# Performance work log

Hardware: AMD Instinct MI355X
Metric: run time of the kernel (lower is better)

The kernel has to match this reference:

```python
import jax, jax.numpy as jnp
import numpy as np

N, E, D, H, ED = 50000, 150000, 128, 4, 16


def _ln(x, g, b, eps=1e-5):
    m = jnp.mean(x, -1, keepdims=True)
    v = jnp.var(x, -1, keepdims=True)
    return (x - m) / jnp.sqrt(v + eps) * g + b


def _seg_softmax(logits, seg, n):
    # numerically stable softmax over edges grouped by destination node
    m = jax.ops.segment_max(logits, seg, num_segments=n)
    e = jnp.exp(logits - m[seg])
    s = jax.ops.segment_sum(e, seg, num_segments=n)
    return e / (s[seg] + 1e-16)


def setup_inputs():
    key = jax.random.key(0)
    ks = jax.random.split(key, 16)
    def w(i, shape, s=0.05):
        return jax.random.normal(ks[i], shape, jnp.float32) * s
    return dict(
        x=w(0, (N, D), 1.0),
        edge_index=jax.random.randint(ks[1], (2, E), 0, N),
        edge_attr=w(2, (E, ED), 1.0),
        sage_Wl=w(3, (D, D)), sage_Wr=w(4, (D, D)), sage_b=jnp.zeros((D,), jnp.float32),
        tq_W=w(5, (D, H * D)), tq_b=jnp.zeros((H * D,), jnp.float32),
        tk_W=w(6, (D, H * D)), tk_b=jnp.zeros((H * D,), jnp.float32),
        tv_W=w(7, (D, H * D)), tv_b=jnp.zeros((H * D,), jnp.float32),
        te_W=w(8, (ED, H * D)),
        tskip_W=w(9, (D, D)), tskip_b=jnp.zeros((D,), jnp.float32),
        gat_W=w(10, (D, H * D)), gat_att_src=w(11, (H, D)), gat_att_dst=w(12, (H, D)),
        gat_bias=jnp.zeros((D,), jnp.float32),
        gate_short=jnp.ones((1,), jnp.float32), gate_attn=jnp.ones((1,), jnp.float32),
        gate_neighbor=jnp.ones((1,), jnp.float32),
        fus_W=w(13, (3 * D, D)), fus_b=jnp.zeros((D,), jnp.float32),
        fus_g=jnp.ones((D,), jnp.float32), fus_beta=jnp.zeros((D,), jnp.float32),
        norm_g=jnp.ones((D,), jnp.float32), norm_b=jnp.zeros((D,), jnp.float32),
    )


def reference(x, edge_index, edge_attr, sage_Wl, sage_Wr, sage_b,
              tq_W, tq_b, tk_W, tk_b, tv_W, tv_b, te_W, tskip_W, tskip_b,
              gat_W, gat_att_src, gat_att_dst, gat_bias,
              gate_short, gate_attn, gate_neighbor,
              fus_W, fus_b, fus_g, fus_beta, norm_g, norm_b):
    n, d = x.shape
    h = tq_W.shape[1] // d
    src, dst = edge_index[0], edge_index[1]

    # --- SAGEConv: mean aggregation of neighbors + root linear ---
    agg = jax.ops.segment_sum(x[src], dst, num_segments=n)
    cnt = jax.ops.segment_sum(jnp.ones((src.shape[0],), x.dtype), dst, num_segments=n)
    mean = agg / jnp.maximum(cnt, 1.0)[:, None]
    x_short = jax.nn.relu(mean @ sage_Wl + x @ sage_Wr + sage_b)

    # --- TransformerConv (concat=False, edge-conditioned key/value, skip) ---
    q = (x @ tq_W + tq_b).reshape(n, h, d)
    k = (x @ tk_W + tk_b).reshape(n, h, d)
    v = (x @ tv_W + tv_b).reshape(n, h, d)
    e = (edge_attr @ te_W).reshape(-1, h, d)           # [E,H,d]
    logits = jnp.sum(q[dst] * (k[src] + e), -1) / np.float32(np.sqrt(d))  # [E,H]
    alpha = _seg_softmax(logits, dst, n)
    out_t = jax.ops.segment_sum((v[src] + e) * alpha[..., None], dst, num_segments=n).mean(1)
    x_attn = jax.nn.relu(out_t + x @ tskip_W + tskip_b)

    # --- GATConv (adds self-loops, concat=False averages heads, bias) ---
    loops = jnp.arange(n)
    s2 = jnp.concatenate([src, loops])
    d2 = jnp.concatenate([dst, loops])
    g = (x @ gat_W).reshape(n, h, d)
    a_s = jnp.sum(g * gat_att_src, -1)                 # [N,H]
    a_d = jnp.sum(g * gat_att_dst, -1)
    lg = jax.nn.leaky_relu(a_s[s2] + a_d[d2], 0.2)     # [E+N,H]
    al = _seg_softmax(lg, d2, n)
    out_g = jax.ops.segment_sum(g[s2] * al[..., None], d2, num_segments=n).mean(1) + gat_bias
    x_nb = jax.nn.relu(out_g)

    # --- gated fusion + residual LayerNorm ---
    gs = jax.nn.sigmoid(gate_short)
    ga = jax.nn.sigmoid(gate_attn)
    gn = jax.nn.sigmoid(gate_neighbor)
    cat = jnp.concatenate([x_short * gs, x_attn * ga, x_nb * gn], -1)
    fused = jax.nn.relu(_ln(cat @ fus_W + fus_b, fus_g, fus_beta))
    return _ln(x + fused, norm_g, norm_b)
```

## Files before the change

kernel.cpp:

```cpp
#include <hip/hip_runtime.h>
#include <hip/hip_bf16.h>

using bf16 = __hip_bfloat16;
typedef __attribute__((ext_vector_type(8))) short short8;
typedef __attribute__((ext_vector_type(4))) float f32x4;
typedef __attribute__((ext_vector_type(4))) unsigned short u16x4;

__device__ __forceinline__ void store4(bf16* p, float v0, float v1, float v2, float v3) {
    u16x4 pk;
    bf16 h0 = __float2bfloat16(v0); pk[0] = *(unsigned short*)&h0;
    bf16 h1 = __float2bfloat16(v1); pk[1] = *(unsigned short*)&h1;
    bf16 h2 = __float2bfloat16(v2); pk[2] = *(unsigned short*)&h2;
    bf16 h3 = __float2bfloat16(v3); pk[3] = *(unsigned short*)&h3;
    *(u16x4*)p = pk;
}
__device__ __forceinline__ float b2f(short s) { bf16 h; *(short*)&h = s; return __bfloat162float(h); }

__device__ __forceinline__ void ld_lds16(void* lds, const void* g) {
    __builtin_amdgcn_global_load_lds(
        (const __attribute__((address_space(1))) unsigned int*)g,
        (__attribute__((address_space(3))) unsigned int*)lds,
        16, 0, 0);
}

__device__ __forceinline__ size_t pidx(int c, int k, int K) {
    return ((size_t)(((c >> 6) * (K >> 5) + (k >> 5)) * 4 + ((c >> 4) & 3)) * 64
            + (((k >> 3) & 3) * 16 + (c & 15))) * 8 + (k & 7);
}

__global__ __launch_bounds__(256) void zero_ws(unsigned* p, size_t n) {
    size_t i = (size_t)blockIdx.x * 256 + threadIdx.x;
    size_t stride = (size_t)gridDim.x * 256;
    for (; i < n; i += stride) p[i] = 0u;
}

__global__ __launch_bounds__(256) void prep_all(
    const float* __restrict__ x, bf16* __restrict__ x_b,
    bf16* __restrict__ Wt_sage, const float* __restrict__ sage_Wl, const float* __restrict__ sage_Wr,
    bf16* __restrict__ Wt_fus, const float* __restrict__ fus_W,
    const float* __restrict__ gate_s, const float* __restrict__ gate_a, const float* __restrict__ gate_n,
    bf16* __restrict__ Wt_cat, const float* __restrict__ tvW,
    const float* __restrict__ tskipW, const float* __restrict__ teW,
    bf16* __restrict__ Wgag, const float* __restrict__ gatW,
    float* __restrict__ bvsum, const float* __restrict__ tvb, int ND)
{
    const int TP = 128 * 128;
    long i = (long)blockIdx.x * 256 + threadIdx.x;
    long nv = ND >> 3;
    if (i < nv) {
        long b = i * 8;
        f32x4 a0 = *(const f32x4*)(x + b);
        f32x4 a1 = *(const f32x4*)(x + b + 4);
        short8 o;
        #pragma unroll
        for (int j = 0; j < 4; ++j) { bf16 h = __float2bfloat16(a0[j]); o[j] = *(short*)&h; }
        #pragma unroll
        for (int j = 0; j < 4; ++j) { bf16 h = __float2bfloat16(a1[j]); o[4 + j] = *(short*)&h; }
        *(short8*)(x_b + b) = o;
        return;
    }
    i -= nv;
    if (i < TP) { int k = (int)i / 128, c = (int)i % 128; Wt_sage[pidx(c, k, 256)] = __float2bfloat16(sage_Wl[i]); return; }
    i -= TP;
    if (i < TP) { int k = (int)i / 128, c = (int)i % 128; Wt_sage[pidx(c, k + 128, 256)] = __float2bfloat16(sage_Wr[i]); return; }
    i -= TP;
    if (i < 3 * TP) {
        int sseg = (int)(i / TP); int r = (int)(i % TP);
        int k = r / 128, c = r % 128;
        const float* g = sseg == 0 ? gate_s : (sseg == 1 ? gate_a : gate_n);
        float gv = 1.0f / (1.0f + expf(-g[0]));
        Wt_fus[pidx(c, sseg * 128 + k, 384)] = __float2bfloat16(fus_W[(size_t)sseg * TP + r] * gv);
        return;
    }
    i -= 3L * TP;
    if (i < 128L * 704) {
        int d = (int)(i / 704), kk = (int)(i % 704);
        float v;
        if (kk < 512)      { int h = kk >> 7, k = kk & 127; v = 0.25f * tvW[k * 512 + h * 128 + d]; }
        else if (kk < 640) { int k = kk - 512;              v = tskipW[k * 128 + d]; }
        else               { int t = kk - 640; int h = t >> 4, j = t & 15; v = 0.25f * teW[j * 512 + h * 128 + d]; }
        Wt_cat[pidx(d, kk, 704)] = __float2bfloat16(v);
        return;
    }
    i -= 128L * 704;
    if (i < 128L * 512) {
        int d = (int)i >> 9, k = (int)i & 511;
        int h = k >> 7, i2 = k & 127;
        Wgag[pidx(d, k, 512)] = __float2bfloat16(0.25f * gatW[(size_t)i2 * 512 + h * 128 + d]);
        return;
    }
    i -= 128L * 512;
    if (i < 128) {
        int d = (int)i;
        bvsum[d] = 0.25f * (tvb[d] + tvb[128 + d] + tvb[256 + d] + tvb[384 + d]);
    }
}

__global__ __launch_bounds__(128) void build_wbig(
    bf16* __restrict__ Wbig, float* __restrict__ bbig,
    const float* __restrict__ Wq, const float* __restrict__ Wk,
    const float* __restrict__ teW, const float* __restrict__ bq,
    const float* __restrict__ bk, const float* __restrict__ gatW,
    const float* __restrict__ attS, const float* __restrict__ attD)
{
    int c = blockIdx.x;
    int ip = threadIdx.x;
    float acc = 0.f, bacc = 0.f;
    if (c < 512) {
        int h = c >> 7, i2 = c & 127;
        const float* wkrow = Wk + (size_t)i2 * 512 + h * 128;
        const float* wqrow = Wq + (size_t)ip * 512 + h * 128;
        for (int o = 0; o < 128; ++o) acc += wqrow[o] * wkrow[o];
        if (ip == 0) { const float* bqr = bq + h * 128; for (int o = 0; o < 128; ++o) bacc += bqr[o] * wkrow[o]; }
    } else if (c < 576) {
        int t = c - 512; int h = t >> 4, j = t & 15;
        const float* terow = teW + (size_t)j * 512 + h * 128;
        const float* wqrow = Wq + (size_t)ip * 512 + h * 128;
        for (int o = 0; o < 128; ++o) acc += wqrow[o] * terow[o];
        if (ip == 0) { const float* bqr = bq + h * 128; for (int o = 0; o < 128; ++o) bacc += bqr[o] * terow[o]; }
    } else if (c < 580) {
        int h = c - 576;
        const float* bkr = bk + h * 128;
        const float* wqrow = Wq + (size_t)ip * 512 + h * 128;
        for (int o = 0; o < 128; ++o) acc += wqrow[o] * bkr[o];
        if (ip == 0) { const float* bqr = bq + h * 128; for (int o = 0; o < 128; ++o) bacc += bqr[o] * bkr[o]; }
    } else if (c < 584) {
        int h = c - 580;
        const float* ar = attS + h * 128;
        const float* gr = gatW + (size_t)ip * 512 + h * 128;
        for (int d = 0; d < 128; ++d) acc += gr[d] * ar[d];
    } else if (c < 588) {
        int h = c - 584;
        const float* ar = attD + h * 128;
        const float* gr = gatW + (size_t)ip * 512 + h * 128;
        for (int d = 0; d < 128; ++d) acc += gr[d] * ar[d];
    }
    Wbig[pidx(c, ip, 128)] = __float2bfloat16(acc);
    if (ip == 0) bbig[c] = bacc;
}

__global__ __launch_bounds__(256) void k_hist(const int* __restrict__ dst, int* __restrict__ deg_i, int E) {
    int e = blockIdx.x * 256 + threadIdx.x;
    if (e < E) atomicAdd(&deg_i[dst[e]], 1);
}

__global__ __launch_bounds__(256) void k_scan1(
    const int* __restrict__ deg_i, int* __restrict__ loc, int* __restrict__ partial, int N)
{
    __shared__ int sm[256];
    int t = threadIdx.x, i = blockIdx.x * 256 + t;
    int v = (i < N) ? deg_i[i] : 0;
    sm[t] = v;
    __syncthreads();
    for (int off = 1; off < 256; off <<= 1) {
        int add = (t >= off) ? sm[t - off] : 0;
        __syncthreads();
        sm[t] += add;
        __syncthreads();
    }
    if (i < N) loc[i] = sm[t] - v;
    if (t == 255) partial[blockIdx.x] = sm[255];
}

__global__ __launch_bounds__(256) void k_scan2(int* __restrict__ partial, int nb) {
    __shared__ int sm[256];
    int t = threadIdx.x;
    int v = (t < nb) ? partial[t] : 0;
    sm[t] = v;
    __syncthreads();
    for (int off = 1; off < 256; off <<= 1) {
        int add = (t >= off) ? sm[t - off] : 0;
        __syncthreads();
        sm[t] += add;
        __syncthreads();
    }
    if (t < nb) partial[t] = sm[t] - v;
}

__global__ __launch_bounds__(256) void k_scan3(
    const int* __restrict__ loc, const int* __restrict__ partial,
    int* __restrict__ rowptr, int* __restrict__ cursor, int N)
{
    int i = blockIdx.x * 256 + threadIdx.x;
    if (i >= N) return;
    int r = loc[i] + partial[blockIdx.x];
    rowptr[i] = r;
    cursor[i] = r;
}

__global__ __launch_bounds__(256) void k_scatter(
    const int* __restrict__ src, const int* __restrict__ dst,
    int* __restrict__ cursor, int* __restrict__ col_src, int* __restrict__ eidx, int E)
{
    int e = blockIdx.x * 256 + threadIdx.x;
    if (e >= E) return;
    int d = dst[e];
    int pos = atomicAdd(&cursor[d], 1);
    col_src[pos] = src[e];
    eidx[pos] = e;
}

__global__ __launch_bounds__(128) void gemm_wide(
    const bf16* __restrict__ A, const bf16* __restrict__ Wt,
    const float* __restrict__ bias, bf16* __restrict__ C, int n_rows, int ldc)
{
    int row0 = blockIdx.x * 64;
    int wave = threadIdx.x >> 6, lane = threadIdx.x & 63;
    int lrow = lane & 15, quad = lane >> 4;
    short8 xb[4][4];
    #pragma unroll
    for (int ks = 0; ks < 4; ++ks)
        #pragma unroll
        for (int nt = 0; nt < 4; ++nt) {
            int r = row0 + nt * 16 + lrow;
            r = r < n_rows ? r : n_rows - 1;
            xb[ks][nt] = *(const short8*)(A + (size_t)r * 128 + ks * 32 + quad * 8);
        }
    int c64 = blockIdx.y * 2 + wave;
    int cbase = c64 * 64;
    f32x4 acc[4][4] = {};
    #pragma unroll
    for (int ks = 0; ks < 4; ++ks) {
        short8 wf[4];
        #pragma unroll
        for (int mt = 0; mt < 4; ++mt)
            wf[mt] = *(const short8*)(Wt + ((size_t)((c64 * 4 + ks) * 4 + mt) * 64 + lane) * 8);
        #pragma unroll
        for (int mt = 0; mt < 4; ++mt)
            #pragma unroll
            for (int nt = 0; nt < 4; ++nt)
                acc[mt][nt] = __builtin_amdgcn_mfma_f32_16x16x32_bf16(wf[mt], xb[ks][nt], acc[mt][nt], 0, 0, 0);
    }
    #pragma unroll
    for (int nt = 0; nt < 4; ++nt) {
        int row = row0 + nt * 16 + lrow;
        if (row >= n_rows) continue;
        #pragma unroll
        for (int mt = 0; mt < 4; ++mt) {
            int col = cbase + mt * 16 + quad * 4;
            float b0 = 0.f, b1 = 0.f, b2 = 0.f, b3 = 0.f;
            if (bias) { b0 = bias[col]; b1 = bias[col + 1]; b2 = bias[col + 2]; b3 = bias[col + 3]; }
            store4(&C[(size_t)row * ldc + col],
                   acc[mt][nt][0] + b0, acc[mt][nt][1] + b1,
                   acc[mt][nt][2] + b2, acc[mt][nt][3] + b3);
        }
    }
}

#define NCAP 8
__global__ __launch_bounds__(256) void node_fused(
    const bf16* __restrict__ QT, const bf16* __restrict__ x_b,
    const float* __restrict__ edge_attr,
    const int* __restrict__ rowptr, const int* __restrict__ deg_i,
    const int* __restrict__ col_src, const int* __restrict__ eidx,
    bf16* __restrict__ mean_b, bf16* __restrict__ xa, bf16* __restrict__ ga,
    bf16* __restrict__ ea_b, int N)
{
    __shared__ short8 xS[4][NCAP][16];
    __shared__ float eaS[4][NCAP][16];
    __shared__ float wTs[4][NCAP][4];
    __shared__ float wGs[4][NCAP][4];
    int w = threadIdx.x >> 6, l = threadIdx.x & 63;
    int n = blockIdx.x * 4 + w;
    if (n >= N) return;
    int j = l & 15, g4 = l >> 4;
    int p0 = rowptr[n], dg = deg_i[n];
    const float scale = 0.08838834764831845f;
    float qtF[4][8], qeqL[4], qbL[4], adh[4], ashn[4];
    #pragma unroll
    for (int h = 0; h < 4; ++h) {
        short8 q = *(const short8*)(QT + (size_t)n * 640 + h * 128 + j * 8);
        #pragma unroll
        for (int t = 0; t < 8; ++t) qtF[h][t] = b2f(q[t]);
        qeqL[h] = __bfloat162float(QT[(size_t)n * 640 + 512 + h * 16 + j]);
        qbL[h]  = __bfloat162float(QT[(size_t)n * 640 + 576 + h]);
        ashn[h] = __bfloat162float(QT[(size_t)n * 640 + 580 + h]);
        adh[h]  = __bfloat162float(QT[(size_t)n * 640 + 584 + h]);
    }
    float xn0 = __bfloat162float(x_b[(size_t)n * 128 + l]);
    float xn1 = __bfloat162float(x_b[(size_t)n * 128 + l + 64]);
    float s_t[4], s_g[4], xaacc[8] = {}, gaacc[8];
    float mean0 = 0.f, mean1 = 0.f, eaacc = 0.f;
    #pragma unroll
    for (int h = 0; h < 4; ++h) {
        s_t[h] = 0.f;
        float lgs = ashn[h] + adh[h];
        lgs = lgs > 0.f ? lgs : 0.2f * lgs;
        float e = __expf(lgs);
        s_g[h] = e;
        gaacc[h * 2] = e * xn0; gaacc[h * 2 + 1] = e * xn1;
    }
    for (int c0 = 0; c0 < dg; c0 += NCAP) {
        int cc = min(NCAP, dg - c0);
        for (int it = 0; it < ((cc + 3) >> 2); ++it) {
            int i = it * 4 + g4;
            bool valid = i < cc;
            int s = 0;
            short8 xf = {0, 0, 0, 0, 0, 0, 0, 0};
            float ea_j = 0.f;
            if (valid) {
                s = col_src[p0 + c0 + i];
                int eg = eidx[p0 + c0 + i];
                xf = *(const short8*)(x_b + (size_t)s * 128 + j * 8);
                ea_j = edge_attr[(size_t)eg * 16 + j];
                xS[w][i][j] = xf;
                eaS[w][i][j] = ea_j;
            }
            float xv[8];
            #pragma unroll
            for (int t = 0; t < 8; ++t) xv[t] = b2f(xf[t]);
            float p[4];
            #pragma unroll
            for (int h = 0; h < 4; ++h) {
                float a = ea_j * qeqL[h];
                #pragma unroll
                for (int t = 0; t < 8; ++t) a += xv[t] * qtF[h][t];
                p[h] = a;
            }
            #pragma unroll
            for (int off = 1; off < 16; off <<= 1)
                #pragma unroll
                for (int h = 0; h < 4; ++h)
                    p[h] += __shfl_xor(p[h], off, 64);
            if (valid && j == 0) {
                #pragma unroll
                for (int h = 0; h < 4; ++h) {
                    wTs[w][i][h] = __expf((p[h] + qbL[h]) * scale);
                    float as_s = __bfloat162float(QT[(size_t)s * 640 + 580 + h]);
                    float lg = as_s + adh[h];
                    lg = lg > 0.f ? lg : 0.2f * lg;
                    wGs[w][i][h] = __expf(lg);
                }
            }
        }
        for (int i = 0; i < cc; ++i) {
            const bf16* xr = (const bf16*)&xS[w][i][0];
            float xv0 = __bfloat162float(xr[l]);
            float xv1 = __bfloat162float(xr[l + 64]);
            mean0 += xv0; mean1 += xv1;
            #pragma unroll
            for (int h = 0; h < 4; ++h) {
                float at = wTs[w][i][h], ag = wGs[w][i][h];
                s_t[h] += at; s_g[h] += ag;
                xaacc[h * 2] += at * xv0; xaacc[h * 2 + 1] += at * xv1;
                gaacc[h * 2] += ag * xv0; gaacc[h * 2 + 1] += ag * xv1;
            }
            eaacc += wTs[w][i][g4] * eaS[w][i][j];
        }
    }
    float invd = 1.f / fmaxf((float)dg, 1.f);
    mean_b[(size_t)n * 128 + l]      = __float2bfloat16(mean0 * invd);
    mean_b[(size_t)n * 128 + l + 64] = __float2bfloat16(mean1 * invd);
    #pragma unroll
    for (int h = 0; h < 4; ++h) {
        float it = 1.f / (s_t[h] + 1e-16f);
        xa[(size_t)n * 512 + h * 128 + l]      = __float2bfloat16(xaacc[h * 2] * it);
        xa[(size_t)n * 512 + h * 128 + l + 64] = __float2bfloat16(xaacc[h * 2 + 1] * it);
        float ig = 1.f / (s_g[h] + 1e-16f);
        ga[(size_t)n * 512 + h * 128 + l]      = __float2bfloat16(gaacc[h * 2] * ig);
        ga[(size_t)n * 512 + h * 128 + l + 64] = __float2bfloat16(gaacc[h * 2 + 1] * ig);
    }
    ea_b[(size_t)n * 64 + l] = __float2bfloat16(eaacc / (s_t[g4] + 1e-16f));
}

#define STASH(BIASP, USE_BV) do { \
    _Pragma("unroll") \
    for (int nt = 0; nt < 4; ++nt) { \
        int row_l = nt * 16 + lrow; \
        int sw = (row_l & 7) << 4; \
        float bvf = (USE_BV) ? ((deg_i[rA[nt]] > 0) ? 1.f : 0.f) : 0.f; \
        _Pragma("unroll") \
        for (int mt = 0; mt < 4; ++mt) { \
            int col = cbase + mt * 16 + quad * 4; \
            f32x4 bb = *(const f32x4*)((BIASP) + col); \
            u16x4 pk; \
            _Pragma("unroll") \
            for (int jj = 0; jj < 4; ++jj) { \
                float v = acc[mt][nt][jj] + bb[jj]; \
                if (USE_BV) v += bvf * bvsum[col + jj]; \
                bf16 h = __float2bfloat16(fmaxf(v, 0.f)); \
                pk[jj] = *(unsigned short*)&h; \
            } \
            *(u16x4*)(tileb + row_l * 256 + ((col * 2) ^ sw)) = pk; \
        } \
    } \
} while (0)

__global__ __launch_bounds__(128) void tail_fused(
    const bf16* __restrict__ mean_b, const bf16* __restrict__ x_b,
    const bf16* __restrict__ ga, const bf16* __restrict__ xa,
    const bf16* __restrict__ ea_b, const int* __restrict__ deg_i,
    const float* __restrict__ x,
    const bf16* __restrict__ Wt_sage, const bf16* __restrict__ Wgag,
    const bf16* __restrict__ Wt_cat, const bf16* __restrict__ Wt_fus,
    const float* __restrict__ sage_b, const float* __restrict__ gat_bias,
    const float* __restrict__ tskip_b, const float* __restrict__ bvsum,
    const float* __restrict__ fus_b, const float* __restrict__ fus_g,
    const float* __restrict__ fus_beta, const float* __restrict__ norm_g,
    const float* __restrict__ norm_b,
    float* __restrict__ out, int N)
{
    __shared__ __align__(16) char tileb[64 * 256];
    __shared__ __align__(16) short8 stg[2][2][8][64];
    __shared__ float2 st1[2][64];
    __shared__ float2 st2[2][64];
    int wave = threadIdx.x >> 6, lane = threadIdx.x & 63;
    int lrow = lane & 15, quad = lane >> 4;
    int kq = quad * 8;
    int row0 = blockIdx.x * 64;
    int cbase = wave * 64;
    int rA[4];
    #pragma unroll
    for (int t = 0; t < 4; ++t) {
        int r = row0 + t * 16 + lrow;
        rA[t] = r < N ? r : N - 1;
    }
    f32x4 facc[4][4] = {};

    auto issueA = [&](const bf16* base, int ldA, int kA, int par) {
        #pragma unroll
        for (int t = 0; t < 4; ++t)
            ld_lds16(&stg[wave][par][t][0], base + (size_t)rA[t] * ldA + kA);
    };
    auto issueW = [&](const bf16* Wt, int stepIdx, int par) {
        #pragma unroll
        for (int mt = 0; mt < 4; ++mt)
            ld_lds16(&stg[wave][par][4 + mt][0], Wt + ((size_t)(stepIdx * 4 + mt) * 64 + lane) * 8);
    };
    auto mfstep = [&](f32x4 (&acc)[4][4], int par) {
        short8 xf[4], wf[4];
        #pragma unroll
        for (int t = 0; t < 4; ++t) { xf[t] = stg[wave][par][t][lane]; wf[t] = stg[wave][par][4 + t][lane]; }
        #pragma unroll
        for (int mt = 0; mt < 4; ++mt)
            #pragma unroll
            for (int nt = 0; nt < 4; ++nt)
                acc[mt][nt] = __builtin_amdgcn_mfma_f32_16x16x32_bf16(wf[mt], xf[nt], acc[mt][nt], 0, 0, 0);
    };
    auto fuse_seg = [&](int SEG) {
        issueW(Wt_fus, wave * 12 + SEG * 4, 0);
        issueW(Wt_fus, wave * 12 + SEG * 4 + 1, 1);
        #pragma unroll
        for (int ks = 0; ks < 4; ++ks) {
            int cur = ks & 1;
            if (ks < 3) asm volatile("s_waitcnt vmcnt(4)" ::: "memory");
            else        asm volatile("s_waitcnt vmcnt(0)" ::: "memory");
            int kT = ks * 32 + kq;
            short8 xf[4], wf[4];
            #pragma unroll
            for (int t = 0; t < 4; ++t) {
                int row_l = t * 16 + lrow;
                xf[t] = *(const short8*)(tileb + row_l * 256 + ((kT * 2) ^ ((row_l & 7) << 4)));
            }
            #pragma unroll
            for (int mt = 0; mt < 4; ++mt) wf[mt] = stg[wave][cur][4 + mt][lane];
            #pragma unroll
            for (int mt = 0; mt < 4; ++mt)
                #pragma unroll
                for (int nt = 0; nt < 4; ++nt)
                    facc[mt][nt] = __builtin_amdgcn_mfma_f32_16x16x32_bf16(wf[mt], xf[nt], facc[mt][nt], 0, 0, 0);
            if (ks + 2 < 4) {
                asm volatile("s_waitcnt lgkmcnt(0)" ::: "memory");
                issueW(Wt_fus, wave * 12 + SEG * 4 + ks + 2, cur);
            }
        }
    };

    {
        f32x4 acc[4][4] = {};
        issueA(mean_b, 128, kq, 0);
        issueW(Wt_sage, wave * 8, 0);
        issueA(mean_b, 128, 32 + kq, 1);
        issueW(Wt_sage, wave * 8 + 1, 1);
        #pragma unroll
        for (int ks = 0; ks < 8; ++ks) {
            int cur = ks & 1;
            if (ks < 7) asm volatile("s_waitcnt vmcnt(8)" ::: "memory");
            else        asm volatile("s_waitcnt vmcnt(0)" ::: "memory");
            mfstep(acc, cur);
            if (ks + 2 < 8) {
                asm volatile("s_waitcnt lgkmcnt(0)" ::: "memory");
                int p = ks + 2;
                issueA((p < 4) ? mean_b : x_b, 128, (p & 3) * 32 + kq, cur);
                issueW(Wt_sage, wave * 8 + p, cur);
            }
        }
        STASH(sage_b, 0);
    }
    __syncthreads();
    fuse_seg(0);
    __syncthreads();

    {
        f32x4 acc[4][4] = {};
        issueA(xa, 512, kq, 0);
        issueW(Wt_cat, wave * 22, 0);
        issueA(xa, 512, 32 + kq, 1);
        issueW(Wt_cat, wave * 22 + 1, 1);
        #pragma unroll
        for (int ks = 0; ks < 22; ++ks) {
            int cur = ks & 1;
            if (ks < 21) asm volatile("s_waitcnt vmcnt(8)" ::: "memory");
            else         asm volatile("s_waitcnt vmcnt(0)" ::: "memory");
            mfstep(acc, cur);
            if (ks + 2 < 22) {
                asm volatile("s_waitcnt lgkmcnt(0)" ::: "memory");
                int p = ks + 2;
                if (p < 16)      issueA(xa,   512, p * 32 + kq,        cur);
                else if (p < 20) issueA(x_b,  128, (p - 16) * 32 + kq, cur);
                else             issueA(ea_b,  64, (p - 20) * 32 + kq, cur);
                issueW(Wt_cat, wave * 22 + p, cur);
            }
        }
        STASH(tskip_b, 1);
    }
    __syncthreads();
    fuse_seg(1);
    __syncthreads();

    {
        f32x4 acc[4][4] = {};
        issueA(ga, 512, kq, 0);
        issueW(Wgag, wave * 16, 0);
        issueA(ga, 512, 32 + kq, 1);
        issueW(Wgag, wave * 16 + 1, 1);
        #pragma unroll
        for (int ks = 0; ks < 16; ++ks) {
            int cur = ks & 1;
            if (ks < 15) asm volatile("s_waitcnt vmcnt(8)" ::: "memory");
            else         asm volatile("s_waitcnt vmcnt(0)" ::: "memory");
            mfstep(acc, cur);
            if (ks + 2 < 16) {
                asm volatile("s_waitcnt lgkmcnt(0)" ::: "memory");
                int p = ks + 2;
                issueA(ga, 512, p * 32 + kq, cur);
                issueW(Wgag, wave * 16 + p, cur);
            }
        }
        STASH(gat_bias, 0);
    }
    __syncthreads();
    fuse_seg(2);

    #pragma unroll
    for (int nt = 0; nt < 4; ++nt) {
        float s = 0.f, q = 0.f;
        #pragma unroll
        for (int mt = 0; mt < 4; ++mt) {
            int col = cbase + mt * 16 + quad * 4;
            f32x4 bb = *(const f32x4*)(fus_b + col);
            #pragma unroll
            for (int jj = 0; jj < 4; ++jj) {
                float v = facc[mt][nt][jj] + bb[jj];
                facc[mt][nt][jj] = v;
                s += v; q += v * v;
            }
        }
        s += __shfl_xor(s, 16, 64); q += __shfl_xor(q, 16, 64);
        s += __shfl_xor(s, 32, 64); q += __shfl_xor(q, 32, 64);
        if (quad == 0) st1[wave][nt * 16 + lrow] = make_float2(s, q);
    }
    __syncthreads();
    float m1[4], inv1[4];
    #pragma unroll
    for (int nt = 0; nt < 4; ++nt) {
        float2 a = st1[0][nt * 16 + lrow], b = st1[1][nt * 16 + lrow];
        float S = a.x + b.x, Q = a.y + b.y;
        float m = S * (1.f / 128.f);
        m1[nt] = m;
        inv1[nt] = rsqrtf(Q * (1.f / 128.f) - m * m + 1e-5f);
    }
    #pragma unroll
    for (int nt = 0; nt < 4; ++nt) {
        float s = 0.f, q = 0.f;
        #pragma unroll
        for (int mt = 0; mt < 4; ++mt) {
            int col = cbase + mt * 16 + quad * 4;
            f32x4 gv = *(const f32x4*)(fus_g + col);
            f32x4 bv = *(const f32x4*)(fus_beta + col);
            f32x4 xv = *(const f32x4*)(x + (size_t)rA[nt] * 128 + col);
            #pragma unroll
            for (int jj = 0; jj < 4; ++jj) {
                float y = fmaxf((facc[mt][nt][jj] - m1[nt]) * inv1[nt] * gv[jj] + bv[jj], 0.f);
                float z = xv[jj] + y;
                facc[mt][nt][jj] = z;
                s += z; q += z * z;
            }
        }
        s += __shfl_xor(s, 16, 64); q += __shfl_xor(q, 16, 64);
        s += __shfl_xor(s, 32, 64); q += __shfl_xor(q, 32, 64);
        if (quad == 0) st2[wave][nt * 16 + lrow] = make_float2(s, q);
    }
    __syncthreads();
    #pragma unroll
    for (int nt = 0; nt < 4; ++nt) {
        int row = row0 + nt * 16 + lrow;
        if (row >= N) continue;
        float2 a = st2[0][nt * 16 + lrow], b = st2[1][nt * 16 + lrow];
        float S = a.x + b.x, Q = a.y + b.y;
        float m = S * (1.f / 128.f);
        float inv = rsqrtf(Q * (1.f / 128.f) - m * m + 1e-5f);
        #pragma unroll
        for (int mt = 0; mt < 4; ++mt) {
            int col = cbase + mt * 16 + quad * 4;
            f32x4 ngv = *(const f32x4*)(norm_g + col);
            f32x4 nbv = *(const f32x4*)(norm_b + col);
            f32x4 o;
            #pragma unroll
            for (int jj = 0; jj < 4; ++jj)
                o[jj] = (facc[mt][nt][jj] - m) * inv * ngv[jj] + nbv[jj];
            *(f32x4*)(out + (size_t)row * 128 + col) = o;
        }
    }
}

extern "C" void kernel_launch(void* const* d_in, const int* in_sizes, int n_in,
                              void* d_out, int out_size, void* d_ws, size_t ws_size,
                              hipStream_t stream)
{
    const float* x        = (const float*)d_in[0];
    const int*   ei       = (const int*)d_in[1];
    const float* edge_attr= (const float*)d_in[2];
    const float* sage_Wl  = (const float*)d_in[3];
    const float* sage_Wr  = (const float*)d_in[4];
    const float* sage_b   = (const float*)d_in[5];
    const float* tq_W     = (const float*)d_in[6];
    const float* tq_b     = (const float*)d_in[7];
    const float* tk_W     = (const float*)d_in[8];
    const float* tk_b     = (const float*)d_in[9];
    const float* tv_W     = (const float*)d_in[10];
    const float* tv_b     = (const float*)d_in[11];
    const float* te_W     = (const float*)d_in[12];
    const float* tskip_W  = (const float*)d_in[13];
    const float* tskip_b  = (const float*)d_in[14];
    const float* gat_W    = (const float*)d_in[15];
    const float* att_s_w  = (const float*)d_in[16];
    const float* att_d_w  = (const float*)d_in[17];
    const float* gat_bias = (const float*)d_in[18];
    const float* gate_s   = (const float*)d_in[19];
    const float* gate_a   = (const float*)d_in[20];
    const float* gate_n   = (const float*)d_in[21];
    const float* fus_W    = (const float*)d_in[22];
    const float* fus_b    = (const float*)d_in[23];
    const float* fus_g    = (const float*)d_in[24];
    const float* fus_beta = (const float*)d_in[25];
    const float* norm_g   = (const float*)d_in[26];
    const float* norm_b   = (const float*)d_in[27];

    int N = in_sizes[0] / 128;
    int E = in_sizes[2] / 16;
    const int* src = ei;
    const int* dst = ei + E;
    int ND = N * 128;
    int nb = (N + 255) / 256;

    char* wsb = (char*)d_ws;
    size_t off = 0;
    auto carve = [&](size_t bytes) -> char* {
        char* p = wsb + off;
        off += (bytes + 255) & ~(size_t)255;
        return p;
    };
    int*   deg_i   = (int*)carve((size_t)N * 4);
    size_t zero_bytes = off;
    int*   rowptr  = (int*)carve((size_t)N * 4);
    int*   cursor  = (int*)carve((size_t)N * 4);
    int*   loc     = (int*)carve((size_t)N * 4);
    int*   partial = (int*)carve((size_t)256 * 4);
    int*   col_src = (int*)carve((size_t)E * 4);
    int*   eidx    = (int*)carve((size_t)E * 4);
    bf16*  x_b     = (bf16*)carve((size_t)N * 128 * 2);
    bf16*  QT      = (bf16*)carve((size_t)N * 640 * 2);
    bf16*  xa      = (bf16*)carve((size_t)N * 512 * 2);
    bf16*  ga      = (bf16*)carve((size_t)N * 512 * 2);
    bf16*  mean_b  = (bf16*)carve((size_t)N * 128 * 2);
    bf16*  ea_b    = (bf16*)carve((size_t)N * 64 * 2);
    bf16*  Wbig    = (bf16*)carve((size_t)640 * 128 * 2);
    float* bbig    = (float*)carve((size_t)640 * 4);
    bf16*  Wt_sage = (bf16*)carve((size_t)128 * 256 * 2);
    bf16*  Wt_fus  = (bf16*)carve((size_t)128 * 384 * 2);
    bf16*  Wt_cat  = (bf16*)carve((size_t)128 * 704 * 2);
    bf16*  Wgag    = (bf16*)carve((size_t)128 * 512 * 2);
    float* bvsum   = (float*)carve((size_t)128 * 4);

    zero_ws<<<256, 256, 0, stream>>>((unsigned*)wsb, zero_bytes / 4);
    const long TP = 128 * 128;
    long prep_total = (long)(ND >> 3) + 5L * TP + 128L * 704 + 128L * 512 + 128;
    int prep_blocks = (int)((prep_total + 255) / 256);
    prep_all<<<prep_blocks, 256, 0, stream>>>(
        x, x_b, Wt_sage, sage_Wl, sage_Wr, Wt_fus, fus_W, gate_s, gate_a, gate_n,
        Wt_cat, tv_W, tskip_W, te_W, Wgag, gat_W, bvsum, tv_b, ND);
    build_wbig<<<640, 128, 0, stream>>>(Wbig, bbig, tq_W, tk_W, te_W, tq_b, tk_b,
                                        gat_W, att_s_w, att_d_w);

    k_hist<<<(E + 255) / 256, 256, 0, stream>>>(dst, deg_i, E);
    k_scan1<<<nb, 256, 0, stream>>>(deg_i, loc, partial, N);
    k_scan2<<<1, 256, 0, stream>>>(partial, nb);
    k_scan3<<<nb, 256, 0, stream>>>(loc, partial, rowptr, cursor, N);
    k_scatter<<<(E + 255) / 256, 256, 0, stream>>>(src, dst, cursor, col_src, eidx, E);

    int gy64 = (N + 63) / 64, gnode = (N + 3) / 4;

    gemm_wide<<<dim3(gy64, 5), 128, 0, stream>>>(x_b, Wbig, bbig, QT, N, 640);

    node_fused<<<gnode, 256, 0, stream>>>(QT, x_b, edge_attr, rowptr, deg_i, col_src, eidx,
                                          mean_b, xa, ga, ea_b, N);

    tail_fused<<<gy64, 128, 0, stream>>>(
        mean_b, x_b, ga, xa, ea_b, deg_i, x,
        Wt_sage, Wgag, Wt_cat, Wt_fus,
        sage_b, gat_bias, tskip_b, bvsum,
        fus_b, fus_g, fus_beta, norm_g, norm_b,
        (float*)d_out, N);
}
```

Before: 373.4 us.

## Merge CSR build into cooperative kernel, fold Wbig into prep, restructure wide GEMM

Folds the build_wbig weight-product computation into prep_all and replaces the five CSR-construction launches (plus the workspace zeroing) with one cooperative kernel that uses grid syncs. This removes launch overhead and inter-kernel gaps. It also changes gemm_wide so each block loops over all five 128-column groups, reusing its x tile and double-buffering weight tiles into LDS with global_load_lds. The trade-off is that the GEMM grid shrinks fivefold, which lowers parallelism, and the cooperative launch needs every block to be co-resident. The zero_ws call now runs only on the fallback path, so any other workspace regions it used to clear may stay uninitialised.

```diff
diff --git a/kernel.cpp b/kernel.cpp
--- a/kernel.cpp
+++ b/kernel.cpp
@@ -1,5 +1,8 @@
 #include <hip/hip_runtime.h>
 #include <hip/hip_bf16.h>
+#include <hip/hip_cooperative_groups.h>
+
+namespace cg = cooperative_groups;
 
 using bf16 = __hip_bfloat16;
 typedef __attribute__((ext_vector_type(8))) short short8;
@@ -42,7 +45,11 @@
     bf16* __restrict__ Wt_cat, const float* __restrict__ tvW,
     const float* __restrict__ tskipW, const float* __restrict__ teW,
     bf16* __restrict__ Wgag, const float* __restrict__ gatW,
-    float* __restrict__ bvsum, const float* __restrict__ tvb, int ND)
+    float* __restrict__ bvsum, const float* __restrict__ tvb,
+    bf16* __restrict__ Wbig, float* __restrict__ bbig,
+    const float* __restrict__ Wq, const float* __restrict__ Wk,
+    const float* __restrict__ bq, const float* __restrict__ bk,
+    const float* __restrict__ attS, const float* __restrict__ attD, int ND)
 {
     const int TP = 128 * 128;
     long i = (long)blockIdx.x * 256 + threadIdx.x;
@@ -93,63 +100,62 @@
     if (i < 128) {
         int d = (int)i;
         bvsum[d] = 0.25f * (tvb[d] + tvb[128 + d] + tvb[256 + d] + tvb[384 + d]);
-    }
-}
-
-__global__ __launch_bounds__(128) void build_wbig(
-    bf16* __restrict__ Wbig, float* __restrict__ bbig,
-    const float* __restrict__ Wq, const float* __restrict__ Wk,
-    const float* __restrict__ teW, const float* __restrict__ bq,
-    const float* __restrict__ bk, const float* __restrict__ gatW,
-    const float* __restrict__ attS, const float* __restrict__ attD)
-{
-    int c = blockIdx.x;
-    int ip = threadIdx.x;
-    float acc = 0.f, bacc = 0.f;
-    if (c < 512) {
-        int h = c >> 7, i2 = c & 127;
-        const float* wkrow = Wk + (size_t)i2 * 512 + h * 128;
-        const float* wqrow = Wq + (size_t)ip * 512 + h * 128;
-        for (int o = 0; o < 128; ++o) acc += wqrow[o] * wkrow[o];
-        if (ip == 0) { const float* bqr = bq + h * 128; for (int o = 0; o < 128; ++o) bacc += bqr[o] * wkrow[o]; }
-    } else if (c < 576) {
-        int t = c - 512; int h = t >> 4, j = t & 15;
-        const float* terow = teW + (size_t)j * 512 + h * 128;
-        const float* wqrow = Wq + (size_t)ip * 512 + h * 128;
-        for (int o = 0; o < 128; ++o) acc += wqrow[o] * terow[o];
-        if (ip == 0) { const float* bqr = bq + h * 128; for (int o = 0; o < 128; ++o) bacc += bqr[o] * terow[o]; }
-    } else if (c < 580) {
-        int h = c - 576;
-        const float* bkr = bk + h * 128;
-        const float* wqrow = Wq + (size_t)ip * 512 + h * 128;
-        for (int o = 0; o < 128; ++o) acc += wqrow[o] * bkr[o];
-        if (ip == 0) { const float* bqr = bq + h * 128; for (int o = 0; o < 128; ++o) bacc += bqr[o] * bkr[o]; }
-    } else if (c < 584) {
-        int h = c - 580;
-        const float* ar = attS + h * 128;
-        const float* gr = gatW + (size_t)ip * 512 + h * 128;
-        for (int d = 0; d < 128; ++d) acc += gr[d] * ar[d];
-    } else if (c < 588) {
-        int h = c - 584;
-        const float* ar = attD + h * 128;
-        const float* gr = gatW + (size_t)ip * 512 + h * 128;
-        for (int d = 0; d < 128; ++d) acc += gr[d] * ar[d];
-    }
-    Wbig[pidx(c, ip, 128)] = __float2bfloat16(acc);
-    if (ip == 0) bbig[c] = bacc;
-}
-
-__global__ __launch_bounds__(256) void k_hist(const int* __restrict__ dst, int* __restrict__ deg_i, int E) {
-    int e = blockIdx.x * 256 + threadIdx.x;
-    if (e < E) atomicAdd(&deg_i[dst[e]], 1);
-}
-
-__global__ __launch_bounds__(256) void k_scan1(
-    const int* __restrict__ deg_i, int* __restrict__ loc, int* __restrict__ partial, int N)
-{
+        return;
+    }
+    i -= 128;
+    if (i < 640L * 128) {
+        int c = (int)(i >> 7), ip = (int)(i & 127);
+        float acc = 0.f, bacc = 0.f;
+        if (c < 512) {
+            int h = c >> 7, i2 = c & 127;
+            const float* wkrow = Wk + (size_t)i2 * 512 + h * 128;
+            const float* wqrow = Wq + (size_t)ip * 512 + h * 128;
+            for (int o = 0; o < 128; ++o) acc += wqrow[o] * wkrow[o];
+            if (ip == 0) { const float* bqr = bq + h * 128; for (int o = 0; o < 128; ++o) bacc += bqr[o] * wkrow[o]; }
+        } else if (c < 576) {
+            int t = c - 512; int h = t >> 4, j = t & 15;
+            const float* terow = teW + (size_t)j * 512 + h * 128;
+            const float* wqrow = Wq + (size_t)ip * 512 + h * 128;
+            for (int o = 0; o < 128; ++o) acc += wqrow[o] * terow[o];
+            if (ip == 0) { const float* bqr = bq + h * 128; for (int o = 0; o < 128; ++o) bacc += bqr[o] * terow[o]; }
+        } else if (c < 580) {
+            int h = c - 576;
+            const float* bkr = bk + h * 128;
+            const float* wqrow = Wq + (size_t)ip * 512 + h * 128;
+            for (int o = 0; o < 128; ++o) acc += wqrow[o] * bkr[o];
+            if (ip == 0) { const float* bqr = bq + h * 128; for (int o = 0; o < 128; ++o) bacc += bqr[o] * bkr[o]; }
+        } else if (c < 584) {
+            int h = c - 580;
+            const float* ar = attS + h * 128;
+            const float* gr = gatW + (size_t)ip * 512 + h * 128;
+            for (int d = 0; d < 128; ++d) acc += gr[d] * ar[d];
+        } else if (c < 588) {
+            int h = c - 584;
+            const float* ar = attD + h * 128;
+            const float* gr = gatW + (size_t)ip * 512 + h * 128;
+            for (int d = 0; d < 128; ++d) acc += gr[d] * ar[d];
+        }
+        Wbig[pidx(c, ip, 128)] = __float2bfloat16(acc);
+        if (ip == 0) bbig[c] = bacc;
+    }
+}
+
+__global__ __launch_bounds__(256) void csr_all(
+    const int* __restrict__ src, const int* __restrict__ dst,
+    int* __restrict__ deg_i, int* __restrict__ rowptr, int* __restrict__ cursor,
+    int* __restrict__ partial, int* __restrict__ col_src, int* __restrict__ eidx,
+    int N, int E)
+{
+    cg::grid_group grid = cg::this_grid();
     __shared__ int sm[256];
-    int t = threadIdx.x, i = blockIdx.x * 256 + t;
-    int v = (i < N) ? deg_i[i] : 0;
+    int t = threadIdx.x, bid = blockIdx.x;
+    int tid = bid * 256 + t;
+    int nth = gridDim.x * 256;
+    for (int i = tid; i < N; i += nth) deg_i[i] = 0;
+    grid.sync();
+    for (int e = tid; e < E; e += nth) atomicAdd(&deg_i[dst[e]], 1);
+    grid.sync();
+    int v = (tid < N) ? deg_i[tid] : 0;
     sm[t] = v;
     __syncthreads();
     for (int off = 1; off < 256; off <<= 1) {
@@ -158,10 +164,58 @@
         sm[t] += add;
         __syncthreads();
     }
+    int loc = sm[t] - v;
+    if (t == 255) partial[bid] = sm[255];
+    grid.sync();
+    if (bid == 0) {
+        int nb = gridDim.x;
+        int pv = (t < nb) ? partial[t] : 0;
+        sm[t] = pv;
+        __syncthreads();
+        for (int off = 1; off < 256; off <<= 1) {
+            int add = (t >= off) ? sm[t - off] : 0;
+            __syncthreads();
+            sm[t] += add;
+            __syncthreads();
+        }
+        if (t < nb) partial[t] = sm[t] - pv;
+    }
+    grid.sync();
+    if (tid < N) {
+        int r = loc + partial[bid];
+        rowptr[tid] = r;
+        cursor[tid] = r;
+    }
+    grid.sync();
+    for (int e = tid; e < E; e += nth) {
+        int d = dst[e];
+        int pos = atomicAdd(&cursor[d], 1);
+        col_src[pos] = src[e];
+        eidx[pos] = e;
+    }
+}
+
+__global__ __launch_bounds__(256) void k_hist(const int* __restrict__ dst, int* __restrict__ deg_i, int E) {
+    int e = blockIdx.x * 256 + threadIdx.x;
+    if (e < E) atomicAdd(&deg_i[dst[e]], 1);
+}
+__global__ __launch_bounds__(256) void k_scan1(
+    const int* __restrict__ deg_i, int* __restrict__ loc, int* __restrict__ partial, int N)
+{
+    __shared__ int sm[256];
+    int t = threadIdx.x, i = blockIdx.x * 256 + t;
+    int v = (i < N) ? deg_i[i] : 0;
+    sm[t] = v;
+    __syncthreads();
+    for (int off = 1; off < 256; off <<= 1) {
+        int add = (t >= off) ? sm[t - off] : 0;
+        __syncthreads();
+        sm[t] += add;
+        __syncthreads();
+    }
     if (i < N) loc[i] = sm[t] - v;
     if (t == 255) partial[blockIdx.x] = sm[255];
 }
-
 __global__ __launch_bounds__(256) void k_scan2(int* __restrict__ partial, int nb) {
     __shared__ int sm[256];
     int t = threadIdx.x;
@@ -176,7 +230,6 @@
     }
     if (t < nb) partial[t] = sm[t] - v;
 }
-
 __global__ __launch_bounds__(256) void k_scan3(
     const int* __restrict__ loc, const int* __restrict__ partial,
     int* __restrict__ rowptr, int* __restrict__ cursor, int N)
@@ -187,7 +240,6 @@
     rowptr[i] = r;
     cursor[i] = r;
 }
-
 __global__ __launch_bounds__(256) void k_scatter(
     const int* __restrict__ src, const int* __restrict__ dst,
     int* __restrict__ cursor, int* __restrict__ col_src, int* __restrict__ eidx, int E)
@@ -204,6 +256,7 @@
     const bf16* __restrict__ A, const bf16* __restrict__ Wt,
     const float* __restrict__ bias, bf16* __restrict__ C, int n_rows, int ldc)
 {
+    __shared__ __align__(16) short8 wstg[2][2][4][64];
     int row0 = blockIdx.x * 64;
     int wave = threadIdx.x >> 6, lane = threadIdx.x & 63;
     int lrow = lane & 15, quad = lane >> 4;
@@ -216,33 +269,47 @@
             r = r < n_rows ? r : n_rows - 1;
             xb[ks][nt] = *(const short8*)(A + (size_t)r * 128 + ks * 32 + quad * 8);
         }
-    int c64 = blockIdx.y * 2 + wave;
-    int cbase = c64 * 64;
-    f32x4 acc[4][4] = {};
-    #pragma unroll
-    for (int ks = 0; ks < 4; ++ks) {
-        short8 wf[4];
+    auto issueW = [&](int s, int par) {
+        int c64 = (s >> 2) * 2 + wave, ks = s & 3;
         #pragma unroll
         for (int mt = 0; mt < 4; ++mt)
-            wf[mt] = *(const short8*)(Wt + ((size_t)((c64 * 4 + ks) * 4 + mt) * 64 + lane) * 8);
-        #pragma unroll
-        for (int mt = 0; mt < 4; ++mt)
-            #pragma unroll
-            for (int nt = 0; nt < 4; ++nt)
-                acc[mt][nt] = __builtin_amdgcn_mfma_f32_16x16x32_bf16(wf[mt], xb[ks][nt], acc[mt][nt], 0, 0, 0);
-    }
-    #pragma unroll
-    for (int nt = 0; nt < 4; ++nt) {
-        int row = row0 + nt * 16 + lrow;
-        if (row >= n_rows) continue;
-        #pragma unroll
-        for (int mt = 0; mt < 4; ++mt) {
-            int col = cbase + mt * 16 + quad * 4;
-            float b0 = 0.f, b1 = 0.f, b2 = 0.f, b3 = 0.f;
-            if (bias) { b0 = bias[col]; b1 = bias[col + 1]; b2 = bias[col + 2]; b3 = bias[col + 3]; }
-            store4(&C[(size_t)row * ldc + col],
-                   acc[mt][nt][0] + b0, acc[mt][nt][1] + b1,
-                   acc[mt][nt][2] + b2, acc[mt][nt][3] + b3);
+            ld_lds16(&wstg[wave][par][mt][0], Wt + ((size_t)((c64 * 4 + ks) * 4 + mt) * 64 + lane) * 8);
+    };
+    issueW(0, 0);
+    issueW(1, 1);
+    for (int cy = 0; cy < 5; ++cy) {
+        f32x4 acc[4][4] = {};
+        #pragma unroll
+        for (int ks = 0; ks < 4; ++ks) {
+            int s = cy * 4 + ks, par = s & 1;
+            if (s < 18) asm volatile("s_waitcnt vmcnt(4)" ::: "memory");
+            else        asm volatile("s_waitcnt vmcnt(0)" ::: "memory");
+            short8 wf[4];
+            #pragma unroll
+            for (int mt = 0; mt < 4; ++mt) wf[mt] = wstg[wave][par][mt][lane];
+            asm volatile("s_waitcnt lgkmcnt(0)" ::: "memory");
+            if (s + 2 < 20) issueW(s + 2, par);
+            __builtin_amdgcn_sched_barrier(0);
+            #pragma unroll
+            for (int mt = 0; mt < 4; ++mt)
+                #pragma unroll
+                for (int nt = 0; nt < 4; ++nt)
+                    acc[mt][nt] = __builtin_amdgcn_mfma_f32_16x16x32_bf16(wf[mt], xb[ks][nt], acc[mt][nt], 0, 0, 0);
+        }
+        int cbase = (cy * 2 + wave) * 64;
+        #pragma unroll
+        for (int nt = 0; nt < 4; ++nt) {
+            int row = row0 + nt * 16 + lrow;
+            if (row >= n_rows) continue;
+            #pragma unroll
+            for (int mt = 0; mt < 4; ++mt) {
+                int col = cbase + mt * 16 + quad * 4;
+                float b0 = 0.f, b1 = 0.f, b2 = 0.f, b3 = 0.f;
+                if (bias) { b0 = bias[col]; b1 = bias[col + 1]; b2 = bias[col + 2]; b3 = bias[col + 3]; }
+                store4(&C[(size_t)row * ldc + col],
+                       acc[mt][nt][0] + b0, acc[mt][nt][1] + b1,
+                       acc[mt][nt][2] + b2, acc[mt][nt][3] + b3);
+            }
         }
     }
 }
@@ -683,25 +750,31 @@
     bf16*  Wgag    = (bf16*)carve((size_t)128 * 512 * 2);
     float* bvsum   = (float*)carve((size_t)128 * 4);
 
-    zero_ws<<<256, 256, 0, stream>>>((unsigned*)wsb, zero_bytes / 4);
     const long TP = 128 * 128;
-    long prep_total = (long)(ND >> 3) + 5L * TP + 128L * 704 + 128L * 512 + 128;
+    long prep_total = (long)(ND >> 3) + 5L * TP + 128L * 704 + 128L * 512 + 128 + 640L * 128;
     int prep_blocks = (int)((prep_total + 255) / 256);
     prep_all<<<prep_blocks, 256, 0, stream>>>(
         x, x_b, Wt_sage, sage_Wl, sage_Wr, Wt_fus, fus_W, gate_s, gate_a, gate_n,
-        Wt_cat, tv_W, tskip_W, te_W, Wgag, gat_W, bvsum, tv_b, ND);
-    build_wbig<<<640, 128, 0, stream>>>(Wbig, bbig, tq_W, tk_W, te_W, tq_b, tk_b,
-                                        gat_W, att_s_w, att_d_w);
-
-    k_hist<<<(E + 255) / 256, 256, 0, stream>>>(dst, deg_i, E);
-    k_scan1<<<nb, 256, 0, stream>>>(deg_i, loc, partial, N);
-    k_scan2<<<1, 256, 0, stream>>>(partial, nb);
-    k_scan3<<<nb, 256, 0, stream>>>(loc, partial, rowptr, cursor, N);
-    k_scatter<<<(E + 255) / 256, 256, 0, stream>>>(src, dst, cursor, col_src, eidx, E);
+        Wt_cat, tv_W, tskip_W, te_W, Wgag, gat_W, bvsum, tv_b,
+        Wbig, bbig, tq_W, tk_W, tq_b, tk_b, att_s_w, att_d_w, ND);
+
+    if (nb <= 256) {
+        void* cargs[] = {(void*)&src, (void*)&dst, (void*)&deg_i, (void*)&rowptr,
+                         (void*)&cursor, (void*)&partial, (void*)&col_src,
+                         (void*)&eidx, (void*)&N, (void*)&E};
+        hipLaunchCooperativeKernel((void*)csr_all, dim3(nb), dim3(256), cargs, 0, stream);
+    } else {
+        zero_ws<<<256, 256, 0, stream>>>((unsigned*)wsb, zero_bytes / 4);
+        k_hist<<<(E + 255) / 256, 256, 0, stream>>>(dst, deg_i, E);
+        k_scan1<<<nb, 256, 0, stream>>>(deg_i, loc, partial, N);
+        k_scan2<<<1, 256, 0, stream>>>(partial, nb);
+        k_scan3<<<nb, 256, 0, stream>>>(loc, partial, rowptr, cursor, N);
+        k_scatter<<<(E + 255) / 256, 256, 0, stream>>>(src, dst, cursor, col_src, eidx, E);
+    }
 
     int gy64 = (N + 63) / 64, gnode = (N + 3) / 4;
 
-    gemm_wide<<<dim3(gy64, 5), 128, 0, stream>>>(x_b, Wbig, bbig, QT, N, 640);
+    gemm_wide<<<gy64, 128, 0, stream>>>(x_b, Wbig, bbig, QT, N, 640);
 
     node_fused<<<gnode, 256, 0, stream>>>(QT, x_b, edge_attr, rowptr, deg_i, col_src, eidx,
                                           mean_b, xa, ga, ea_b, N);
```

Result: slower. 512.8 us (+37.3%).
